# Kernel tuning notes

Hardware: AMD Instinct MI355X
Metric: run time of the kernel (lower is better)

Reference implementation:

```python
import jax, jax.numpy as jnp
import numpy as np

B, HID, NUM_RIS = 65536, 256, 64
R = NUM_RIS // 4  # number of 4-qubit circuit runs


def _cnot_perm(c, t):
    # basis index i has wire 0 as most-significant bit (matches shape (2,2,2,2) row-major)
    idx = np.arange(16)
    cbit = (idx >> (3 - c)) & 1
    return idx ^ (cbit << (3 - t))

P01 = jnp.asarray(_cnot_perm(0, 1))
P23 = jnp.asarray(_cnot_perm(2, 3))
P12 = jnp.asarray(_cnot_perm(1, 2))
P30 = jnp.asarray(_cnot_perm(3, 0))


def apply_ry(state, theta, wire):
    # state: (B, R, 2,2,2,2); theta broadcastable to (B, R)
    ax = 2 + wire
    c = jnp.cos(theta * 0.5)[..., None, None, None]
    s = jnp.sin(theta * 0.5)[..., None, None, None]
    s0 = jnp.take(state, 0, axis=ax)
    s1 = jnp.take(state, 1, axis=ax)
    return jnp.stack([c * s0 - s * s1, s * s0 + c * s1], axis=ax)


def apply_cnot(state, perm):
    b, r = state.shape[:2]
    return state.reshape(b, r, 16)[:, :, perm].reshape(b, r, 2, 2, 2, 2)


def setup_inputs() -> dict:
    key = jax.random.key(0)
    k1, k2, k3 = jax.random.split(key, 3)
    fused = jax.random.normal(k1, (B, HID), dtype=jnp.float32)
    W_proj = jax.random.normal(k2, (4 * R, HID), dtype=jnp.float32) * (1.0 / np.sqrt(HID))
    b_proj = jnp.zeros((4 * R,), dtype=jnp.float32)
    vqc_weights = jax.random.normal(k3, (R, 4, 4), dtype=jnp.float32) * 0.01
    return {"fused": fused, "W_proj": W_proj, "b_proj": b_proj, "vqc_weights": vqc_weights}


def reference(fused, W_proj, b_proj, vqc_weights):
    b = fused.shape[0]
    r = vqc_weights.shape[0]
    angles = jnp.tanh(fused @ W_proj.T + b_proj) * jnp.pi  # (B, 4R)
    angles = angles.reshape(b, r, 4)

    # initial |0000> state, batched over (B, R)
    state = jnp.zeros((b, r, 2, 2, 2, 2), dtype=fused.dtype).at[:, :, 0, 0, 0, 0].set(1.0)

    # input encoding layer
    for w in range(4):
        state = apply_ry(state, angles[:, :, w], w)
    # variational layer 0 + entanglers
    for w in range(4):
        state = apply_ry(state, vqc_weights[:, 0, w][None], w)
    state = apply_cnot(state, P01)
    state = apply_cnot(state, P23)
    # layer 1
    for w in range(4):
        state = apply_ry(state, vqc_weights[:, 1, w][None], w)
    state = apply_cnot(state, P12)
    state = apply_cnot(state, P30)
    # layer 2
    for w in range(4):
        state = apply_ry(state, vqc_weights[:, 2, w][None], w)
    state = apply_cnot(state, P01)
    state = apply_cnot(state, P12)
    state = apply_cnot(state, P23)
    state = apply_cnot(state, P30)
    # layer 3
    for w in range(4):
        state = apply_ry(state, vqc_weights[:, 3, w][None], w)

    # <Z_w> = sum(p | bit_w=0) - sum(p | bit_w=1)
    prob = state * state  # RY/CNOT keep state real
    evs = []
    for w in range(4):
        ax = 2 + w
        diff = jnp.take(prob, 0, axis=ax) - jnp.take(prob, 1, axis=ax)
        evs.append(diff.sum(axis=(2, 3, 4)))  # (B, R)
    z = jnp.stack(evs, axis=-1).reshape(b, r * 4)  # matches torch.cat over runs
    return (z + 1.0) * jnp.pi
```

## Files before the change

### kernel.cpp

```cpp
#include <hip/hip_runtime.h>
#include <math.h>


#define PI_F 3.14159265358979323846f

typedef _Float16 f16x4 __attribute__((ext_vector_type(4)));
typedef _Float16 f16x8 __attribute__((ext_vector_type(8)));
typedef float    f32x4 __attribute__((ext_vector_type(4)));
typedef float    f32x16 __attribute__((ext_vector_type(16)));

__device__ __forceinline__ void ry_gate(float st[16], float c, float s, int w) {
    const int m = 1 << (3 - w);
    #pragma unroll
    for (int i = 0; i < 16; ++i) {
        if (i & m) continue;
        float a = st[i];
        float b = st[i | m];
        st[i]     = c * a - s * b;
        st[i | m] = s * a + c * b;
    }
}

__device__ __forceinline__ void cnot_gate(float st[16], int cw, int tw) {
    const int cm = 1 << (3 - cw);
    const int tm = 1 << (3 - tw);
    #pragma unroll
    for (int i = 0; i < 16; ++i) {
        if ((i & cm) && !(i & tm)) {
            float tmp = st[i];
            st[i] = st[i | tm];
            st[i | tm] = tmp;
        }
    }
}

__global__ void prep_kernel(const float* __restrict__ vw,
                            const float* __restrict__ W,
                            char* __restrict__ ws) {
    const int tid = threadIdx.x;
    if (blockIdx.x == 0) {
        float* Ut = (float*)(ws + 49152);
        {
            const int r = tid >> 4, j = tid & 15;
            const float* wr = vw + r * 16;
            float cs[16], sn[16];
            #pragma unroll
            for (int i = 0; i < 16; ++i) {
                float h = wr[i] * 0.5f;
                cs[i] = __cosf(h);
                sn[i] = __sinf(h);
            }
            float st[16];
            #pragma unroll
            for (int i = 0; i < 16; ++i) st[i] = 0.f;
            st[j] = 1.f;
            #pragma unroll
            for (int w = 0; w < 4; ++w) ry_gate(st, cs[w], sn[w], w);
            cnot_gate(st, 0, 1);
            cnot_gate(st, 2, 3);
            #pragma unroll
            for (int w = 0; w < 4; ++w) ry_gate(st, cs[4 + w], sn[4 + w], w);
            cnot_gate(st, 1, 2);
            cnot_gate(st, 3, 0);
            #pragma unroll
            for (int w = 0; w < 4; ++w) ry_gate(st, cs[8 + w], sn[8 + w], w);
            cnot_gate(st, 0, 1);
            cnot_gate(st, 1, 2);
            cnot_gate(st, 2, 3);
            cnot_gate(st, 3, 0);
            #pragma unroll
            for (int w = 0; w < 4; ++w) ry_gate(st, cs[12 + w], sn[12 + w], w);
            #pragma unroll
            for (int i = 0; i < 16; ++i) Ut[r * 256 + i * 16 + j] = st[i];
        }
        __syncthreads();
        {
            _Float16* UA = (_Float16*)(ws + 32768);
            #pragma unroll
            for (int t = 0; t < 4; ++t) {
                int f = t * 256 + tid;
                int r = f >> 6, lane = f & 63;
                int i = lane & 31, hh = lane >> 5;
                const float* urow = Ut + r * 256 + (i & 15) * 16;
                f16x8 h;
                #pragma unroll
                for (int e = 0; e < 8; ++e) {
                    float u = urow[8 * hh + e];
                    if (i < 16) {
                        h[e] = (_Float16)u;
                    } else {
                        _Float16 hi = (_Float16)u;
                        h[e] = (_Float16)(u - (float)hi);
                    }
                }
                *(f16x8*)(UA + f * 8) = h;
            }
        }
    } else {
        _Float16* Wh = (_Float16*)ws;
        #pragma unroll
        for (int t = 0; t < 8; ++t) {
            int f  = tid * 8 + t;
            int cg = f >> 9;
            int kk = (f >> 6) & 7;
            int l  = f & 63;
            int row = cg * 16 + (l & 15);
            int k0  = (kk * 4 + (l >> 4)) * 8;
            const float* src = W + row * 256 + k0;
            f16x8 h;
            #pragma unroll
            for (int e = 0; e < 8; ++e) h[e] = (_Float16)src[e];
            *(f16x8*)(Wh + f * 8) = h;
        }
    }
}

__global__ __launch_bounds__(256, 3) void vqc_main_kernel(
        const float* __restrict__ fused,
        const char* __restrict__ ws,
        const float* __restrict__ bp,
        float* __restrict__ out) {
    __shared__ __align__(16) char smem[16384 + 16 * 32 * 16];

    const int tid  = threadIdx.x;
    const int lane = tid & 63;
    const int cg   = tid >> 6;
    const int l15  = lane & 15;
    const int l4   = lane >> 4;
    const size_t b0 = (size_t)blockIdx.x * 32;

    const f16x8* Wf = (const f16x8*)ws;
    f16x8 af[8];
    #pragma unroll
    for (int kk = 0; kk < 8; ++kk) af[kk] = Wf[(cg * 8 + kk) * 64 + lane];

    const f16x8* UA = (const f16x8*)(ws + 32768);
    f16x8 ua[4];
    #pragma unroll
    for (int rr = 0; rr < 4; ++rr) ua[rr] = UA[(4 * cg + rr) * 64 + lane];

    float4 bb = *(const float4*)(bp + 4 * (4 * cg + l4));

    {
        const float4* s4 = (const float4*)(fused + b0 * 256);
        #pragma unroll
        for (int it = 0; it < 8; ++it) {
            int q = tid + it * 256;
            float4 v = s4[q];
            int row = q >> 6;
            int c4  = (q & 63) << 2;
            int sl  = (c4 >> 3) ^ (row & 7);
            int byteoff = row * 512 + (sl << 4) + ((c4 & 7) << 1);
            f16x4 h = { (_Float16)v.x, (_Float16)v.y, (_Float16)v.z, (_Float16)v.w };
            *(f16x4*)(smem + byteoff) = h;
        }
    }
    __syncthreads();

    f32x4 acc[2] = {};
    #pragma unroll
    for (int kk = 0; kk < 8; ++kk) {
        int slot = kk * 4 + l4;
        #pragma unroll
        for (int sg = 0; sg < 2; ++sg) {
            int frow = sg * 16 + l15;
            f16x8 bf = *(const f16x8*)(smem + frow * 512 + ((slot ^ (frow & 7)) << 4));
            acc[sg] = __builtin_amdgcn_mfma_f32_16x16x32_f16(af[kk], bf, acc[sg], 0, 0, 0);
        }
    }

    _Float16* tab = (_Float16*)(smem + 16384);
    const int r_own = 4 * cg + l4;
    #pragma unroll
    for (int sg = 0; sg < 2; ++sg) {
        float bias[4] = {bb.x, bb.y, bb.z, bb.w};
        float cc[4], ssn[4];
        #pragma unroll
        for (int w = 0; w < 4; ++w) {
            float pre = acc[sg][w] + bias[w];
            float e   = __expf(2.f * pre);
            float th  = __fdividef(e - 1.f, e + 1.f);
            float hh  = th * (0.5f * PI_F);
            __sincosf(hh, &ssn[w], &cc[w]);
        }
        f16x8 t;
        t[0] = (_Float16)(cc[0] * cc[1]);  t[1] = (_Float16)(cc[0] * ssn[1]);
        t[2] = (_Float16)(ssn[0] * cc[1]); t[3] = (_Float16)(ssn[0] * ssn[1]);
        t[4] = (_Float16)(cc[2] * cc[3]);  t[5] = (_Float16)(cc[2] * ssn[3]);
        t[6] = (_Float16)(ssn[2] * cc[3]); t[7] = (_Float16)(ssn[2] * ssn[3]);
        *(f16x8*)(tab + (r_own * 32 + sg * 16 + l15) * 8) = t;
    }

    const int   s  = lane & 31;
    const int   hh = lane >> 5;
    const float g1 = hh ? -1.f : 1.f;

    #pragma unroll
    for (int rr = 0; rr < 4; ++rr) {
        const int r = 4 * cg + rr;
        f16x8 t = *(const f16x8*)(tab + (r * 32 + s) * 8);
        _Float16 a0 = t[2 * hh], a1 = t[2 * hh + 1];
        f16x8 se;
        se[0] = a0 * t[4]; se[1] = a0 * t[5];
        se[2] = a0 * t[6]; se[3] = a0 * t[7];
        se[4] = a1 * t[4]; se[5] = a1 * t[5];
        se[6] = a1 * t[6]; se[7] = a1 * t[7];

        f32x16 zero = {};
        f32x16 o = __builtin_amdgcn_mfma_f32_32x32x16_f16(ua[rr], se, zero, 0, 0, 0);

        float p[8];
        #pragma unroll
        for (int j = 0; j < 8; ++j) {
            float of = o[j] + o[j + 8];
            p[j] = of * of;
        }
        float a = p[0] + p[1], b = p[2] + p[3];
        float c = p[4] + p[5], d = p[6] + p[7];
        float ab = a + b, cd = c + d;
        float z0 = ab - cd;
        float z1 = g1 * (ab + cd);
        float z2 = (a - b) + (c - d);
        float z3 = (p[0] - p[1] + p[2] - p[3]) + (p[4] - p[5] + p[6] - p[7]);

        z0 += __shfl_xor(z0, 32);
        z1 += __shfl_xor(z1, 32);
        z2 += __shfl_xor(z2, 32);
        z3 += __shfl_xor(z3, 32);

        if (hh == 0) {
            float4 ov;
            ov.x = (z0 + 1.f) * PI_F;
            ov.y = (z1 + 1.f) * PI_F;
            ov.z = (z2 + 1.f) * PI_F;
            ov.w = (z3 + 1.f) * PI_F;
            *(float4*)(out + (b0 + s) * 64 + 4 * r) = ov;
        }
    }
}

extern "C" void kernel_launch(void* const* d_in, const int* in_sizes, int n_in,
                              void* d_out, int out_size, void* d_ws, size_t ws_size,
                              hipStream_t stream) {
    const float* fused = (const float*)d_in[0];
    const float* Wp    = (const float*)d_in[1];
    const float* bp    = (const float*)d_in[2];
    const float* vw    = (const float*)d_in[3];
    float* out = (float*)d_out;
    char*  ws  = (char*)d_ws;

    prep_kernel<<<2, 256, 0, stream>>>(vw, Wp, ws);

    const int B = 65536;
    vqc_main_kernel<<<B / 32, 256, 0, stream>>>(fused, ws, bp, out);
}
```

Before: 26.63 us.

## Make main kernel persistent over four tiles with register-prefetched input

Each block now handles four 32-row tiles instead of one, loading the next tile's fused rows into registers while the current tile's MFMA and quantum-circuit work runs. The W and U fragments held in registers are then loaded once per four tiles. Launch bounds are raised to 4 waves per SIMD. The risks are the extra 32 registers for staging, an added barrier per tile, and a grid of only 512 blocks, which may leave some CUs with little work.

```diff
diff --git a/kernel.cpp b/kernel.cpp
--- a/kernel.cpp
+++ b/kernel.cpp
@@ -115,7 +115,9 @@
     }
 }
 
-__global__ __launch_bounds__(256, 3) void vqc_main_kernel(
+#define NT 4
+
+__global__ __launch_bounds__(256, 4) void vqc_main_kernel(
         const float* __restrict__ fused,
         const char* __restrict__ ws,
         const float* __restrict__ bp,
@@ -127,7 +129,6 @@
     const int cg   = tid >> 6;
     const int l15  = lane & 15;
     const int l4   = lane >> 4;
-    const size_t b0 = (size_t)blockIdx.x * 32;
 
     const f16x8* Wf = (const f16x8*)ws;
     f16x8 af[8];
@@ -141,12 +142,30 @@
 
     float4 bb = *(const float4*)(bp + 4 * (4 * cg + l4));
 
+    float4 stg[8];
     {
-        const float4* s4 = (const float4*)(fused + b0 * 256);
+        const float4* s4 = (const float4*)(fused + (size_t)blockIdx.x * NT * 8192);
+        #pragma unroll
+        for (int it = 0; it < 8; ++it) stg[it] = s4[tid + it * 256];
+    }
+
+    _Float16* tab = (_Float16*)(smem + 16384);
+    const int r_own = 4 * cg + l4;
+    const int s32   = lane & 31;
+    const int hh    = lane >> 5;
+    const float g1  = hh ? -1.f : 1.f;
+
+    #pragma unroll 1
+    for (int t = 0; t < NT; ++t) {
+        const size_t tb = (size_t)blockIdx.x * NT + t;
+        const size_t b0 = tb * 32;
+
+        if (t > 0) __syncthreads();
+
         #pragma unroll
         for (int it = 0; it < 8; ++it) {
             int q = tid + it * 256;
-            float4 v = s4[q];
+            float4 v = stg[it];
             int row = q >> 6;
             int c4  = (q & 63) << 2;
             int sl  = (c4 >> 3) ^ (row & 7);
@@ -154,87 +173,88 @@
             f16x4 h = { (_Float16)v.x, (_Float16)v.y, (_Float16)v.z, (_Float16)v.w };
             *(f16x4*)(smem + byteoff) = h;
         }
-    }
-    __syncthreads();
-
-    f32x4 acc[2] = {};
-    #pragma unroll
-    for (int kk = 0; kk < 8; ++kk) {
-        int slot = kk * 4 + l4;
+
+        if (t + 1 < NT) {
+            const float4* s4 = (const float4*)(fused + (tb + 1) * 8192);
+            #pragma unroll
+            for (int it = 0; it < 8; ++it) stg[it] = s4[tid + it * 256];
+        }
+
+        __syncthreads();
+
+        f32x4 acc[2] = {};
+        #pragma unroll
+        for (int kk = 0; kk < 8; ++kk) {
+            int slot = kk * 4 + l4;
+            #pragma unroll
+            for (int sg = 0; sg < 2; ++sg) {
+                int frow = sg * 16 + l15;
+                f16x8 bf = *(const f16x8*)(smem + frow * 512 + ((slot ^ (frow & 7)) << 4));
+                acc[sg] = __builtin_amdgcn_mfma_f32_16x16x32_f16(af[kk], bf, acc[sg], 0, 0, 0);
+            }
+        }
+
         #pragma unroll
         for (int sg = 0; sg < 2; ++sg) {
-            int frow = sg * 16 + l15;
-            f16x8 bf = *(const f16x8*)(smem + frow * 512 + ((slot ^ (frow & 7)) << 4));
-            acc[sg] = __builtin_amdgcn_mfma_f32_16x16x32_f16(af[kk], bf, acc[sg], 0, 0, 0);
-        }
-    }
-
-    _Float16* tab = (_Float16*)(smem + 16384);
-    const int r_own = 4 * cg + l4;
-    #pragma unroll
-    for (int sg = 0; sg < 2; ++sg) {
-        float bias[4] = {bb.x, bb.y, bb.z, bb.w};
-        float cc[4], ssn[4];
-        #pragma unroll
-        for (int w = 0; w < 4; ++w) {
-            float pre = acc[sg][w] + bias[w];
-            float e   = __expf(2.f * pre);
-            float th  = __fdividef(e - 1.f, e + 1.f);
-            float hh  = th * (0.5f * PI_F);
-            __sincosf(hh, &ssn[w], &cc[w]);
-        }
-        f16x8 t;
-        t[0] = (_Float16)(cc[0] * cc[1]);  t[1] = (_Float16)(cc[0] * ssn[1]);
-        t[2] = (_Float16)(ssn[0] * cc[1]); t[3] = (_Float16)(ssn[0] * ssn[1]);
-        t[4] = (_Float16)(cc[2] * cc[3]);  t[5] = (_Float16)(cc[2] * ssn[3]);
-        t[6] = (_Float16)(ssn[2] * cc[3]); t[7] = (_Float16)(ssn[2] * ssn[3]);
-        *(f16x8*)(tab + (r_own * 32 + sg * 16 + l15) * 8) = t;
-    }
-
-    const int   s  = lane & 31;
-    const int   hh = lane >> 5;
-    const float g1 = hh ? -1.f : 1.f;
-
-    #pragma unroll
-    for (int rr = 0; rr < 4; ++rr) {
-        const int r = 4 * cg + rr;
-        f16x8 t = *(const f16x8*)(tab + (r * 32 + s) * 8);
-        _Float16 a0 = t[2 * hh], a1 = t[2 * hh + 1];
-        f16x8 se;
-        se[0] = a0 * t[4]; se[1] = a0 * t[5];
-        se[2] = a0 * t[6]; se[3] = a0 * t[7];
-        se[4] = a1 * t[4]; se[5] = a1 * t[5];
-        se[6] = a1 * t[6]; se[7] = a1 * t[7];
-
-        f32x16 zero = {};
-        f32x16 o = __builtin_amdgcn_mfma_f32_32x32x16_f16(ua[rr], se, zero, 0, 0, 0);
-
-        float p[8];
-        #pragma unroll
-        for (int j = 0; j < 8; ++j) {
-            float of = o[j] + o[j + 8];
-            p[j] = of * of;
-        }
-        float a = p[0] + p[1], b = p[2] + p[3];
-        float c = p[4] + p[5], d = p[6] + p[7];
-        float ab = a + b, cd = c + d;
-        float z0 = ab - cd;
-        float z1 = g1 * (ab + cd);
-        float z2 = (a - b) + (c - d);
-        float z3 = (p[0] - p[1] + p[2] - p[3]) + (p[4] - p[5] + p[6] - p[7]);
-
-        z0 += __shfl_xor(z0, 32);
-        z1 += __shfl_xor(z1, 32);
-        z2 += __shfl_xor(z2, 32);
-        z3 += __shfl_xor(z3, 32);
-
-        if (hh == 0) {
-            float4 ov;
-            ov.x = (z0 + 1.f) * PI_F;
-            ov.y = (z1 + 1.f) * PI_F;
-            ov.z = (z2 + 1.f) * PI_F;
-            ov.w = (z3 + 1.f) * PI_F;
-            *(float4*)(out + (b0 + s) * 64 + 4 * r) = ov;
+            float bias[4] = {bb.x, bb.y, bb.z, bb.w};
+            float cc[4], ssn[4];
+            #pragma unroll
+            for (int w = 0; w < 4; ++w) {
+                float pre = acc[sg][w] + bias[w];
+                float e   = __expf(2.f * pre);
+                float th  = __fdividef(e - 1.f, e + 1.f);
+                float ha  = th * (0.5f * PI_F);
+                __sincosf(ha, &ssn[w], &cc[w]);
+            }
+            f16x8 tt;
+            tt[0] = (_Float16)(cc[0] * cc[1]);  tt[1] = (_Float16)(cc[0] * ssn[1]);
+            tt[2] = (_Float16)(ssn[0] * cc[1]); tt[3] = (_Float16)(ssn[0] * ssn[1]);
+            tt[4] = (_Float16)(cc[2] * cc[3]);  tt[5] = (_Float16)(cc[2] * ssn[3]);
+            tt[6] = (_Float16)(ssn[2] * cc[3]); tt[7] = (_Float16)(ssn[2] * ssn[3]);
+            *(f16x8*)(tab + (r_own * 32 + sg * 16 + l15) * 8) = tt;
+        }
+
+        #pragma unroll
+        for (int rr = 0; rr < 4; ++rr) {
+            const int r = 4 * cg + rr;
+            f16x8 tt = *(const f16x8*)(tab + (r * 32 + s32) * 8);
+            _Float16 a0 = tt[2 * hh], a1 = tt[2 * hh + 1];
+            f16x8 se;
+            se[0] = a0 * tt[4]; se[1] = a0 * tt[5];
+            se[2] = a0 * tt[6]; se[3] = a0 * tt[7];
+            se[4] = a1 * tt[4]; se[5] = a1 * tt[5];
+            se[6] = a1 * tt[6]; se[7] = a1 * tt[7];
+
+            f32x16 zero = {};
+            f32x16 o = __builtin_amdgcn_mfma_f32_32x32x16_f16(ua[rr], se, zero, 0, 0, 0);
+
+            float p[8];
+            #pragma unroll
+            for (int j = 0; j < 8; ++j) {
+                float of = o[j] + o[j + 8];
+                p[j] = of * of;
+            }
+            float a = p[0] + p[1], b = p[2] + p[3];
+            float c = p[4] + p[5], d = p[6] + p[7];
+            float ab = a + b, cd = c + d;
+            float z0 = ab - cd;
+            float z1 = g1 * (ab + cd);
+            float z2 = (a - b) + (c - d);
+            float z3 = (p[0] - p[1] + p[2] - p[3]) + (p[4] - p[5] + p[6] - p[7]);
+
+            z0 += __shfl_xor(z0, 32);
+            z1 += __shfl_xor(z1, 32);
+            z2 += __shfl_xor(z2, 32);
+            z3 += __shfl_xor(z3, 32);
+
+            if (hh == 0) {
+                float4 ov;
+                ov.x = (z0 + 1.f) * PI_F;
+                ov.y = (z1 + 1.f) * PI_F;
+                ov.z = (z2 + 1.f) * PI_F;
+                ov.w = (z3 + 1.f) * PI_F;
+                *(float4*)(out + (b0 + s32) * 64 + 4 * r) = ov;
+            }
         }
     }
 }
@@ -252,5 +272,5 @@
     prep_kernel<<<2, 256, 0, stream>>>(vw, Wp, ws);
 
     const int B = 65536;
-    vqc_main_kernel<<<B / 32, 256, 0, stream>>>(fused, ws, bp, out);
-}
+    vqc_main_kernel<<<B / (32 * NT), 256, 0, stream>>>(fused, ws, bp, out);
+}
```

Result: slower. 30.83 us (+15.8%).
